# Kernel tuning notes

Hardware: AMD Instinct MI355X
Metric: run time of the kernel (lower is better)

The kernel has to match this reference:

```python
import jax, jax.numpy as jnp
import numpy as np

N_NODES = 100000
N_EDGES = 3200000
N_FEAT = 128
N_CLASSES = 8


def setup_inputs() -> dict:
    key = jax.random.key(0)
    ks = jax.random.split(key, 8)
    h = jax.random.normal(ks[0], (N_NODES, N_FEAT), dtype=jnp.float32)
    edge_index = jax.random.randint(ks[1], (2, N_EDGES), 0, N_NODES, dtype=jnp.int64)
    def lin(k, fi, fo):
        return jax.random.normal(k, (fi, fo), dtype=jnp.float32) / np.sqrt(fi)
    return {
        "h": h,
        "edge_index": edge_index,
        "W1": lin(ks[2], N_FEAT, 16), "b1": jnp.zeros((16,), jnp.float32),
        "W2": lin(ks[3], 16, 4),      "b2": jnp.zeros((4,), jnp.float32),
        "W3": lin(ks[4], 4, 2),      "b3": jnp.zeros((2,), jnp.float32),
        "Wc": lin(ks[5], 2, N_CLASSES), "bc": jnp.zeros((N_CLASSES,), jnp.float32),
    }


def _gcn_norm(edge_index, n_nodes):
    # PyG GCNConv: add self-loops, symmetric normalization deg^-1/2 A deg^-1/2
    loop = jnp.arange(n_nodes, dtype=edge_index.dtype)
    src = jnp.concatenate([edge_index[0], loop])  # [E+N]
    dst = jnp.concatenate([edge_index[1], loop])
    deg = jax.ops.segment_sum(jnp.ones_like(dst, dtype=jnp.float32), dst,
                              num_segments=n_nodes)
    dinv = jnp.where(deg > 0, jax.lax.rsqrt(deg), 0.0)
    norm = dinv[src] * dinv[dst]  # [E+N]
    return src, dst, norm


def _gcn_conv(x, W, b, src, dst, norm, n_nodes):
    xw = x @ W                                # [N, Fo] linear first (small Fo)
    msg = xw[src] * norm[:, None]             # gather + scale  [E+N, Fo]
    out = jax.ops.segment_sum(msg, dst, num_segments=n_nodes)  # scatter-add
    return out + b


def reference(h, edge_index, W1, b1, W2, b2, W3, b3, Wc, bc):
    n = h.shape[0]
    src, dst, norm = _gcn_norm(edge_index, n)
    h1 = jnp.tanh(_gcn_conv(h, W1, b1, src, dst, norm, n))
    h2 = jnp.tanh(_gcn_conv(h1, W2, b2, src, dst, norm, n))
    h3 = jnp.tanh(_gcn_conv(h2, W3, b3, src, dst, norm, n))
    out = h3 @ Wc + bc
    return (out, h3)
```

## Files before the change

kernel.cpp:

```cpp
#include <hip/hip_runtime.h>
#include <math.h>

#define N_NODES 100000
#define N_EDGES 3200000
#define NPB    256
#define NBUCK  ((N_NODES + NPB - 1) / NPB)
#define NBLKA  256
#define EPB    ((N_EDGES + NBLKA - 1) / NBLKA)
#define NB_BLK ((N_NODES + 255) / 256)

#define NEW_WS_WORDS (3u*N_NODES + N_EDGES + 3200000u + NBUCK*NBLKA + NBUCK + 2u)
#define NEW_WS_BYTES (NEW_WS_WORDS * 4u)
#define ATOMIC_WS_BYTES ((33u*N_NODES + 16u) * 4u)

__global__ void k_detect_i64(const int* __restrict__ ei_words, int* __restrict__ flag) {
    if (blockIdx.x == 0 && threadIdx.x == 0) {
        int allzero = 1;
        for (int i = 0; i < 64; i++)
            if (ei_words[2 * i + 1] != 0) allzero = 0;
        *flag = allzero;
    }
}

__device__ __forceinline__ unsigned load_idx(const int* p32, const long long* p64,
                                             int is64, int e) {
    return is64 ? (unsigned)(unsigned long long)p64[e] : (unsigned)p32[e];
}

__global__ __launch_bounds__(256) void k_bcount(const int* __restrict__ dst32,
                                                const long long* __restrict__ dst64,
                                                const int* __restrict__ flag,
                                                int* __restrict__ cmat) {
    __shared__ int lc[NBUCK];
    int t = threadIdx.x, blk = blockIdx.x;
    for (int i = t; i < NBUCK; i += 256) lc[i] = 0;
    __syncthreads();
    int is64 = *flag;
    int e0 = blk * EPB;
    int e1 = e0 + EPB; if (e1 > N_EDGES) e1 = N_EDGES;
    for (int e = e0 + t; e < e1; e += 256) {
        unsigned d = load_idx(dst32, dst64, is64, e);
        if (d < N_NODES) atomicAdd(&lc[d >> 8], 1);
    }
    __syncthreads();
    for (int b = t; b < NBUCK; b += 256) cmat[b * NBLKA + blk] = lc[b];
}

__global__ __launch_bounds__(256) void k_bsum(const int* __restrict__ cmat,
                                              int* __restrict__ bt) {
    int b = blockIdx.x, t = threadIdx.x;
    int v = cmat[b * NBLKA + t];
#pragma unroll
    for (int off = 32; off > 0; off >>= 1) v += __shfl_down(v, off, 64);
    __shared__ int s[4];
    if ((t & 63) == 0) s[t >> 6] = v;
    __syncthreads();
    if (t == 0) bt[b] = s[0] + s[1] + s[2] + s[3];
}

__global__ __launch_bounds__(512) void k_btscan(int* __restrict__ bt) {
    __shared__ int s[512];
    int t = threadIdx.x;
    s[t] = (t < NBUCK) ? bt[t] : 0;
    __syncthreads();
    for (int off = 1; off < 512; off <<= 1) {
        int v = (t >= off) ? s[t - off] : 0;
        __syncthreads();
        s[t] += v;
        __syncthreads();
    }
    if (t < NBUCK) bt[t] = (t == 0) ? 0 : s[t - 1];
    if (t == 0) bt[NBUCK] = s[NBUCK - 1];
}

__global__ __launch_bounds__(256) void k_boffs(int* __restrict__ cmat,
                                               const int* __restrict__ bt) {
    __shared__ int s[256];
    int b = blockIdx.x, t = threadIdx.x;
    int v0 = cmat[b * NBLKA + t];
    s[t] = v0;
    __syncthreads();
    for (int off = 1; off < 256; off <<= 1) {
        int v = (t >= off) ? s[t - off] : 0;
        __syncthreads();
        s[t] += v;
        __syncthreads();
    }
    cmat[b * NBLKA + t] = ((t == 0) ? 0 : s[t - 1]) + bt[b];
}

__global__ __launch_bounds__(256) void k_bscatter(const int* __restrict__ src32,
                                                  const long long* __restrict__ src64,
                                                  const int* __restrict__ dst32,
                                                  const long long* __restrict__ dst64,
                                                  const int* __restrict__ flag,
                                                  const int* __restrict__ cmat,
                                                  int* __restrict__ P) {
    __shared__ int cur[NBUCK];
    int t = threadIdx.x, blk = blockIdx.x;
    for (int i = t; i < NBUCK; i += 256) cur[i] = cmat[i * NBLKA + blk];
    __syncthreads();
    int is64 = *flag;
    int e0 = blk * EPB;
    int e1 = e0 + EPB; if (e1 > N_EDGES) e1 = N_EDGES;
    for (int e = e0 + t; e < e1; e += 256) {
        unsigned d = load_idx(dst32, dst64, is64, e);
        if (d < N_NODES) {
            unsigned s = load_idx(src32, src64, is64, e);
            int pos = atomicAdd(&cur[d >> 8], 1);
            P[pos] = (int)(((d & 255u) << 17) | (s & 0x1FFFFu));
        }
    }
}

__global__ __launch_bounds__(256) void k_bbuild(const int* __restrict__ P,
                                                const int* __restrict__ bt,
                                                int* __restrict__ adj,
                                                int* __restrict__ rowstart,
                                                int* __restrict__ rowend,
                                                float* __restrict__ dinv) {
    __shared__ int cnt[NPB];
    __shared__ int s[NPB];
    int b = blockIdx.x, t = threadIdx.x;
    int bo = bt[b], be = bt[b + 1];
    cnt[t] = 0;
    __syncthreads();
    for (int i = bo + t; i < be; i += 256) atomicAdd(&cnt[P[i] >> 17], 1);
    __syncthreads();
    s[t] = cnt[t];
    __syncthreads();
    for (int off = 1; off < 256; off <<= 1) {
        int v = (t >= off) ? s[t - off] : 0;
        __syncthreads();
        s[t] += v;
        __syncthreads();
    }
    int ex = (t == 0) ? 0 : s[t - 1];
    int node = b * NPB + t;
    if (node < N_NODES) {
        rowstart[node] = bo + ex;
        rowend[node]   = bo + ex + cnt[t];
        dinv[node]     = rsqrtf((float)cnt[t] + 1.0f);
    }
    __syncthreads();
    s[t] = ex;
    __syncthreads();
    for (int i = bo + t; i < be; i += 256) {
        int ent = P[i];
        int pos = bo + atomicAdd(&s[ent >> 17], 1);
        adj[pos] = ent & 0x1FFFF;
    }
}

__global__ __launch_bounds__(256) void k_gemm1(const float* __restrict__ h,
                                               const float* __restrict__ W,
                                               const float* __restrict__ dinv,
                                               float* __restrict__ xs,
                                               float* acc) {
    __shared__ float Wt[16 * 132];
    __shared__ float Hs[16 * 132];
    int tid = threadIdx.x;
    for (int i = tid; i < 2048; i += 256) {
        int k = i >> 4, f = i & 15;
        Wt[f * 132 + k] = W[i];
    }
    int nodeBase = blockIdx.x * 16;
    for (int i = tid; i < 512; i += 256) {
        int r = i >> 5, c = i & 31;
        float4 v = ((const float4*)(h + (size_t)(nodeBase + r) * 128))[c];
        *((float4*)&Hs[r * 132 + c * 4]) = v;
    }
    __syncthreads();
    int nl = tid >> 4;
    int f  = tid & 15;
    int n  = nodeBase + nl;
    const float* hr = &Hs[nl * 132];
    const float* wr = &Wt[f * 132];
    float s = 0.0f;
#pragma unroll
    for (int k = 0; k < 128; k++) s += hr[k] * wr[k];
    s *= dinv[n];
    xs[n * 16 + f]  = s;
    acc[n * 16 + f] = s;
}

template <int FI, int FO>
__global__ __launch_bounds__(256) void k_gemm_small(const float* __restrict__ x,
                                                    const float* __restrict__ W,
                                                    const float* __restrict__ dinv,
                                                    float* __restrict__ xs,
                                                    float* acc) {
    int i = blockIdx.x * 256 + threadIdx.x;
    if (i >= N_NODES * FO) return;
    int n = i / FO, f = i % FO;
    float s = 0.0f;
#pragma unroll
    for (int k = 0; k < FI; k++) s += x[n * FI + k] * W[k * FO + f];
    s *= dinv[n];
    xs[i] = s;
    acc[i] = s;
}

template <int F, int NL>
__global__ __launch_bounds__(256) void k_pull(const float* __restrict__ xs,
                                              const int* __restrict__ adj,
                                              const int* __restrict__ rowstart,
                                              const int* __restrict__ rowend,
                                              const float* __restrict__ dinv,
                                              const float* __restrict__ b,
                                              float* __restrict__ out) {
    constexpr int R = NL / F;
    int t = threadIdx.x;
    int g = t / NL, q = t % NL;
    int f = q % F,  k = q / F;
    int n = blockIdx.x * (256 / NL) + g;
    if (n >= N_NODES) return;
    int s0 = rowstart[n], e0 = rowend[n];
    float acc = 0.0f;
    for (int j = s0 + k; j < e0; j += R)
        acc += xs[adj[j] * F + f];
#pragma unroll
    for (int off = NL / 2; off >= F; off >>= 1)
        acc += __shfl_xor(acc, off, 64);
    if (k == 0) {
        acc += xs[n * F + f];
        out[n * F + f] = tanhf(dinv[n] * acc + b[f]);
    }
}

__global__ __launch_bounds__(256) void k_pull_final(const float* __restrict__ xs,
                                                    const int* __restrict__ adj,
                                                    const int* __restrict__ rowstart,
                                                    const int* __restrict__ rowend,
                                                    const float* __restrict__ dinv,
                                                    const float* __restrict__ b3,
                                                    const float* __restrict__ Wc,
                                                    const float* __restrict__ bc,
                                                    float* __restrict__ out,
                                                    float* __restrict__ h3out) {
    const int NL = 8;
    int t = threadIdx.x;
    int g = t / NL, q = t % NL;
    int f = q & 1, k = q >> 1;
    int n = blockIdx.x * (256 / NL) + g;
    if (n >= N_NODES) return;
    int s0 = rowstart[n], e0 = rowend[n];
    float acc = 0.0f;
    for (int j = s0 + k; j < e0; j += 4)
        acc += xs[adj[j] * 2 + f];
    acc += __shfl_xor(acc, 4, 64);
    acc += __shfl_xor(acc, 2, 64);
    float a = 0.0f;
    if (q < 2) {
        acc += xs[n * 2 + f];
        a = tanhf(dinv[n] * acc + b3[f]);
        h3out[2 * n + f] = a;
    }
    int wl = t & 63, gb = wl & ~7;
    float a0 = __shfl(a, gb, 64);
    float a1 = __shfl(a, gb + 1, 64);
    out[8 * n + q] = a0 * Wc[q] + a1 * Wc[8 + q] + bc[q];
}

template <int F>
__global__ __launch_bounds__(256) void k_scatter(const int* __restrict__ src32,
                                                 const long long* __restrict__ src64,
                                                 const int* __restrict__ dst32,
                                                 const long long* __restrict__ dst64,
                                                 const int* __restrict__ flag,
                                                 const float* __restrict__ xs,
                                                 float* __restrict__ acc) {
    long long gid = (long long)blockIdx.x * 256 + threadIdx.x;
    int e = (int)(gid / F), f = (int)(gid % F);
    if (e < N_EDGES) {
        int is64 = *flag;
        unsigned s = load_idx(src32, src64, is64, e);
        unsigned d = load_idx(dst32, dst64, is64, e);
        if (s < N_NODES && d < N_NODES)
            atomicAdd(&acc[d * F + f], xs[s * F + f]);
    }
}
__global__ __launch_bounds__(256) void k_deg_init(float* __restrict__ deg) {
    int i = blockIdx.x * 256 + threadIdx.x;
    if (i < N_NODES) deg[i] = 1.0f;
}
__global__ __launch_bounds__(256) void k_deg_count(const int* __restrict__ dst32,
                                                   const long long* __restrict__ dst64,
                                                   const int* __restrict__ flag,
                                                   float* __restrict__ deg) {
    int e = blockIdx.x * 256 + threadIdx.x;
    if (e < N_EDGES) {
        unsigned d = load_idx(dst32, dst64, *flag, e);
        if (d < N_NODES) atomicAdd(&deg[d], 1.0f);
    }
}
__global__ __launch_bounds__(256) void k_rsqrt(float* __restrict__ deg) {
    int i = blockIdx.x * 256 + threadIdx.x;
    if (i < N_NODES) deg[i] = rsqrtf(deg[i]);
}
template <int F>
__global__ __launch_bounds__(256) void k_finish(const float* __restrict__ acc,
                                                const float* __restrict__ dinv,
                                                const float* __restrict__ b,
                                                float* __restrict__ out) {
    int i = blockIdx.x * 256 + threadIdx.x;
    if (i >= N_NODES * F) return;
    int n = i / F, f = i % F;
    out[i] = tanhf(dinv[n] * acc[i] + b[f]);
}
__global__ __launch_bounds__(256) void k_final(const float* __restrict__ acc3,
                                               const float* __restrict__ dinv,
                                               const float* __restrict__ b3,
                                               const float* __restrict__ Wc,
                                               const float* __restrict__ bc,
                                               float* __restrict__ out,
                                               float* __restrict__ h3out) {
    int n = blockIdx.x * 256 + threadIdx.x;
    if (n >= N_NODES) return;
    float di = dinv[n];
    float a0 = tanhf(di * acc3[2 * n + 0] + b3[0]);
    float a1 = tanhf(di * acc3[2 * n + 1] + b3[1]);
    h3out[2 * n + 0] = a0;
    h3out[2 * n + 1] = a1;
#pragma unroll
    for (int c = 0; c < 8; c++)
        out[8 * n + c] = a0 * Wc[c] + a1 * Wc[8 + c] + bc[c];
}
__global__ __launch_bounds__(256) void k_zero_out(float* __restrict__ out, int n) {
    int i = blockIdx.x * 256 + threadIdx.x;
    if (i < n) out[i] = 0.0f;
}

extern "C" void kernel_launch(void* const* d_in, const int* in_sizes, int n_in,
                              void* d_out, int out_size, void* d_ws, size_t ws_size,
                              hipStream_t stream) {
    float* out = (float*)d_out;
    const float* h   = (const float*)d_in[0];
    const void*  ei  = d_in[1];
    const float* W1  = (const float*)d_in[2];
    const float* b1  = (const float*)d_in[3];
    const float* W2  = (const float*)d_in[4];
    const float* b2  = (const float*)d_in[5];
    const float* W3  = (const float*)d_in[6];
    const float* b3  = (const float*)d_in[7];
    const float* Wc  = (const float*)d_in[8];
    const float* bc  = (const float*)d_in[9];

    const int*       src32 = (const int*)ei;
    const int*       dst32 = src32 + N_EDGES;
    const long long* src64 = (const long long*)ei;
    const long long* dst64 = src64 + N_EDGES;

    float* h3out = out + 8 * N_NODES;
    const int NB_E = (N_EDGES + 255) / 256;

    if (d_ws != nullptr && ws_size >= NEW_WS_BYTES) {
        float* dinv    = (float*)d_ws;
        int* rowstart  = (int*)(dinv + N_NODES);
        int* rowend    = rowstart + N_NODES;
        int* adj       = rowend + N_NODES;
        int* S         = adj + N_EDGES;
        float* xs      = (float*)S;
        float* hbuf    = xs + 16 * N_NODES;
        int* P         = S;
        int* cmat      = S + 3200000;
        int* bt        = cmat + NBUCK * NBLKA;
        int* flag      = bt + NBUCK + 1;

        k_detect_i64<<<1, 64, 0, stream>>>(src32, flag);
        k_bcount<<<NBLKA, 256, 0, stream>>>(dst32, dst64, flag, cmat);
        k_bsum<<<NBUCK, 256, 0, stream>>>(cmat, bt);
        k_btscan<<<1, 512, 0, stream>>>(bt);
        k_boffs<<<NBUCK, 256, 0, stream>>>(cmat, bt);
        k_bscatter<<<NBLKA, 256, 0, stream>>>(src32, src64, dst32, dst64, flag, cmat, P);
        k_bbuild<<<NBUCK, 256, 0, stream>>>(P, bt, adj, rowstart, rowend, dinv);

        k_gemm1<<<N_NODES / 16, 256, 0, stream>>>(h, W1, dinv, xs, xs);
        k_pull<16, 64><<<(N_NODES * 64 + 255) / 256, 256, 0, stream>>>(
            xs, adj, rowstart, rowend, dinv, b1, hbuf);
        k_gemm_small<16, 4><<<(N_NODES * 4 + 255) / 256, 256, 0, stream>>>(hbuf, W2, dinv, xs, xs);
        k_pull<4, 16><<<(N_NODES * 16 + 255) / 256, 256, 0, stream>>>(
            xs, adj, rowstart, rowend, dinv, b2, hbuf);
        k_gemm_small<4, 2><<<(N_NODES * 2 + 255) / 256, 256, 0, stream>>>(hbuf, W3, dinv, xs, xs);
        k_pull_final<<<(N_NODES * 8 + 255) / 256, 256, 0, stream>>>(
            xs, adj, rowstart, rowend, dinv, b3, Wc, bc, out, h3out);
        return;
    }

    if (d_ws != nullptr && ws_size >= ATOMIC_WS_BYTES) {
        float* ws   = (float*)d_ws;
        float* dinv = ws;
        float* bufA = dinv + N_NODES;
        float* bufB = bufA + 16 * N_NODES;
        int*   flag = (int*)(bufB + 16 * N_NODES);
        float* xs1 = bufA, *acc1 = bufB, *h1 = bufA;
        float* xs2 = bufB, *acc2 = bufB + 4 * N_NODES, *h2 = bufA;
        float* xs3 = bufB, *acc3 = bufB + 2 * N_NODES;

        k_detect_i64<<<1, 64, 0, stream>>>(src32, flag);
        k_deg_init<<<NB_BLK, 256, 0, stream>>>(dinv);
        k_deg_count<<<NB_E, 256, 0, stream>>>(dst32, dst64, flag, dinv);
        k_rsqrt<<<NB_BLK, 256, 0, stream>>>(dinv);
        k_gemm1<<<N_NODES / 16, 256, 0, stream>>>(h, W1, dinv, xs1, acc1);
        k_scatter<16><<<(int)(((long long)N_EDGES * 16 + 255) / 256), 256, 0, stream>>>(
            src32, src64, dst32, dst64, flag, xs1, acc1);
        k_finish<16><<<(N_NODES * 16 + 255) / 256, 256, 0, stream>>>(acc1, dinv, b1, h1);
        k_gemm_small<16, 4><<<(N_NODES * 4 + 255) / 256, 256, 0, stream>>>(h1, W2, dinv, xs2, acc2);
        k_scatter<4><<<(int)(((long long)N_EDGES * 4 + 255) / 256), 256, 0, stream>>>(
            src32, src64, dst32, dst64, flag, xs2, acc2);
        k_finish<4><<<(N_NODES * 4 + 255) / 256, 256, 0, stream>>>(acc2, dinv, b2, h2);
        k_gemm_small<4, 2><<<(N_NODES * 2 + 255) / 256, 256, 0, stream>>>(h2, W3, dinv, xs3, acc3);
        k_scatter<2><<<(int)(((long long)N_EDGES * 2 + 255) / 256), 256, 0, stream>>>(
            src32, src64, dst32, dst64, flag, xs3, acc3);
        k_final<<<NB_BLK, 256, 0, stream>>>(acc3, dinv, b3, Wc, bc, out, h3out);
        return;
    }

    k_zero_out<<<(out_size + 255) / 256, 256, 0, stream>>>(out, out_size);
}
```

Measured before the change: 351.0 us.

## Replace CSR pull with bucketed shared-memory atomic aggregation over packed edges

Drops the per-node CSR build (rowstart/rowend/adj) and aggregates directly from the bucket-sorted packed edge list P. Each block owns 128 destination nodes and accumulates messages with LDS atomics. Layer-1 features are split into two 8-wide planes so the shared accumulator fits, and edge-index and P reads use nontemporal loads. This removes the second sort pass and the irregular row-length imbalance, at the cost of reading P several times (once per layer or plane) and contended LDS atomics.

Result: slower. 738.5 us (+110.4%).

```diff
diff --git a/kernel.cpp b/kernel.cpp
--- a/kernel.cpp
+++ b/kernel.cpp
@@ -3,14 +3,14 @@
 
 #define N_NODES 100000
 #define N_EDGES 3200000
-#define NPB    256
+#define NPB    128
 #define NBUCK  ((N_NODES + NPB - 1) / NPB)
 #define NBLKA  256
 #define EPB    ((N_EDGES + NBLKA - 1) / NBLKA)
 #define NB_BLK ((N_NODES + 255) / 256)
 
-#define NEW_WS_WORDS (3u*N_NODES + N_EDGES + 3200000u + NBUCK*NBLKA + NBUCK + 2u)
-#define NEW_WS_BYTES (NEW_WS_WORDS * 4u)
+#define MAIN_WS_WORDS (33u*N_NODES + N_EDGES + NBUCK*NBLKA + NBUCK + 2u)
+#define MAIN_WS_BYTES (MAIN_WS_WORDS * 4u)
 #define ATOMIC_WS_BYTES ((33u*N_NODES + 16u) * 4u)
 
 __global__ void k_detect_i64(const int* __restrict__ ei_words, int* __restrict__ flag) {
@@ -24,7 +24,8 @@
 
 __device__ __forceinline__ unsigned load_idx(const int* p32, const long long* p64,
                                              int is64, int e) {
-    return is64 ? (unsigned)(unsigned long long)p64[e] : (unsigned)p32[e];
+    return is64 ? (unsigned)(unsigned long long)__builtin_nontemporal_load(&p64[e])
+                : (unsigned)__builtin_nontemporal_load(&p32[e]);
 }
 
 __global__ __launch_bounds__(256) void k_bcount(const int* __restrict__ dst32,
@@ -36,11 +37,10 @@
     for (int i = t; i < NBUCK; i += 256) lc[i] = 0;
     __syncthreads();
     int is64 = *flag;
-    int e0 = blk * EPB;
-    int e1 = e0 + EPB; if (e1 > N_EDGES) e1 = N_EDGES;
+    int e0 = blk * EPB, e1 = e0 + EPB; if (e1 > N_EDGES) e1 = N_EDGES;
     for (int e = e0 + t; e < e1; e += 256) {
         unsigned d = load_idx(dst32, dst64, is64, e);
-        if (d < N_NODES) atomicAdd(&lc[d >> 8], 1);
+        if (d < N_NODES) atomicAdd(&lc[d >> 7], 1);
     }
     __syncthreads();
     for (int b = t; b < NBUCK; b += 256) cmat[b * NBLKA + blk] = lc[b];
@@ -58,12 +58,12 @@
     if (t == 0) bt[b] = s[0] + s[1] + s[2] + s[3];
 }
 
-__global__ __launch_bounds__(512) void k_btscan(int* __restrict__ bt) {
-    __shared__ int s[512];
+__global__ __launch_bounds__(1024) void k_btscan(int* __restrict__ bt) {
+    __shared__ int s[1024];
     int t = threadIdx.x;
     s[t] = (t < NBUCK) ? bt[t] : 0;
     __syncthreads();
-    for (int off = 1; off < 512; off <<= 1) {
+    for (int off = 1; off < 1024; off <<= 1) {
         int v = (t >= off) ? s[t - off] : 0;
         __syncthreads();
         s[t] += v;
@@ -77,8 +77,7 @@
                                                const int* __restrict__ bt) {
     __shared__ int s[256];
     int b = blockIdx.x, t = threadIdx.x;
-    int v0 = cmat[b * NBLKA + t];
-    s[t] = v0;
+    s[t] = cmat[b * NBLKA + t];
     __syncthreads();
     for (int off = 1; off < 256; off <<= 1) {
         int v = (t >= off) ? s[t - off] : 0;
@@ -101,62 +100,38 @@
     for (int i = t; i < NBUCK; i += 256) cur[i] = cmat[i * NBLKA + blk];
     __syncthreads();
     int is64 = *flag;
-    int e0 = blk * EPB;
-    int e1 = e0 + EPB; if (e1 > N_EDGES) e1 = N_EDGES;
+    int e0 = blk * EPB, e1 = e0 + EPB; if (e1 > N_EDGES) e1 = N_EDGES;
     for (int e = e0 + t; e < e1; e += 256) {
         unsigned d = load_idx(dst32, dst64, is64, e);
         if (d < N_NODES) {
             unsigned s = load_idx(src32, src64, is64, e);
-            int pos = atomicAdd(&cur[d >> 8], 1);
-            P[pos] = (int)(((d & 255u) << 17) | (s & 0x1FFFFu));
+            int pos = atomicAdd(&cur[d >> 7], 1);
+            P[pos] = (int)(((d & 127u) << 17) | (s & 0x1FFFFu));
         }
     }
 }
 
-__global__ __launch_bounds__(256) void k_bbuild(const int* __restrict__ P,
-                                                const int* __restrict__ bt,
-                                                int* __restrict__ adj,
-                                                int* __restrict__ rowstart,
-                                                int* __restrict__ rowend,
-                                                float* __restrict__ dinv) {
+__global__ __launch_bounds__(256) void k_bdinv(const int* __restrict__ P,
+                                               const int* __restrict__ bt,
+                                               float* __restrict__ dinv) {
     __shared__ int cnt[NPB];
-    __shared__ int s[NPB];
     int b = blockIdx.x, t = threadIdx.x;
-    int bo = bt[b], be = bt[b + 1];
-    cnt[t] = 0;
-    __syncthreads();
-    for (int i = bo + t; i < be; i += 256) atomicAdd(&cnt[P[i] >> 17], 1);
-    __syncthreads();
-    s[t] = cnt[t];
-    __syncthreads();
-    for (int off = 1; off < 256; off <<= 1) {
-        int v = (t >= off) ? s[t - off] : 0;
-        __syncthreads();
-        s[t] += v;
-        __syncthreads();
-    }
-    int ex = (t == 0) ? 0 : s[t - 1];
-    int node = b * NPB + t;
-    if (node < N_NODES) {
-        rowstart[node] = bo + ex;
-        rowend[node]   = bo + ex + cnt[t];
-        dinv[node]     = rsqrtf((float)cnt[t] + 1.0f);
-    }
-    __syncthreads();
-    s[t] = ex;
-    __syncthreads();
-    for (int i = bo + t; i < be; i += 256) {
-        int ent = P[i];
-        int pos = bo + atomicAdd(&s[ent >> 17], 1);
-        adj[pos] = ent & 0x1FFFF;
-    }
-}
-
-__global__ __launch_bounds__(256) void k_gemm1(const float* __restrict__ h,
-                                               const float* __restrict__ W,
-                                               const float* __restrict__ dinv,
-                                               float* __restrict__ xs,
-                                               float* acc) {
+    for (int i = t; i < NPB; i += 256) cnt[i] = 0;
+    __syncthreads();
+    int s0 = bt[b], s1 = bt[b + 1];
+    for (int j = s0 + t; j < s1; j += 256)
+        atomicAdd(&cnt[__builtin_nontemporal_load(&P[j]) >> 17], 1);
+    __syncthreads();
+    for (int i = t; i < NPB; i += 256) {
+        int n = b * NPB + i;
+        if (n < N_NODES) dinv[n] = rsqrtf((float)cnt[i] + 1.0f);
+    }
+}
+
+__global__ __launch_bounds__(256) void k_gemm1_p(const float* __restrict__ h,
+                                                 const float* __restrict__ W,
+                                                 const float* __restrict__ dinv,
+                                                 float* __restrict__ xs) {
     __shared__ float Wt[16 * 132];
     __shared__ float Hs[16 * 132];
     int tid = threadIdx.x;
@@ -171,25 +146,136 @@
         *((float4*)&Hs[r * 132 + c * 4]) = v;
     }
     __syncthreads();
-    int nl = tid >> 4;
-    int f  = tid & 15;
-    int n  = nodeBase + nl;
+    int nl = tid >> 4, f = tid & 15;
+    int n = nodeBase + nl;
     const float* hr = &Hs[nl * 132];
     const float* wr = &Wt[f * 132];
     float s = 0.0f;
 #pragma unroll
     for (int k = 0; k < 128; k++) s += hr[k] * wr[k];
     s *= dinv[n];
-    xs[n * 16 + f]  = s;
+    xs[(f >> 3) * (8 * N_NODES) + n * 8 + (f & 7)] = s;
+}
+
+template <int FI, int FO>
+__global__ __launch_bounds__(256) void k_gemm_smallp(const float* __restrict__ x,
+                                                     const float* __restrict__ W,
+                                                     const float* __restrict__ dinv,
+                                                     float* __restrict__ xs) {
+    int i = blockIdx.x * 256 + threadIdx.x;
+    if (i >= N_NODES * FO) return;
+    int n = i / FO, f = i % FO;
+    float s = 0.0f;
+#pragma unroll
+    for (int k = 0; k < FI; k++) s += x[n * FI + k] * W[k * FO + f];
+    xs[i] = s * dinv[n];
+}
+
+template <int F, int FTOT, int FOFF, int LOG>
+__global__ __launch_bounds__(256) void k_agg(const int* __restrict__ P,
+                                             const int* __restrict__ bt,
+                                             const float* __restrict__ xsp,
+                                             const float* __restrict__ dinv,
+                                             const float* __restrict__ bias,
+                                             float* __restrict__ out) {
+    __shared__ float acc[NPB * F];
+    int b = blockIdx.x, t = threadIdx.x;
+    for (int i = t; i < NPB * F; i += 256) acc[i] = 0.0f;
+    __syncthreads();
+    int s0 = bt[b], s1 = bt[b + 1];
+    int sub = t & (F - 1);
+    for (int j = s0 + (t >> LOG); j < s1; j += (256 >> LOG)) {
+        int ent = __builtin_nontemporal_load(&P[j]);
+        int src = ent & 0x1FFFF;
+        int dl  = ent >> 17;
+        atomicAdd(&acc[dl * F + sub], xsp[src * F + sub]);
+    }
+    __syncthreads();
+    for (int i = t; i < NPB * F; i += 256) {
+        int n = b * NPB + (i >> LOG);
+        if (n < N_NODES) {
+            int fl = i & (F - 1);
+            float a = acc[i] + xsp[n * F + fl];
+            out[n * FTOT + FOFF + fl] = tanhf(dinv[n] * a + bias[fl]);
+        }
+    }
+}
+
+__global__ __launch_bounds__(256) void k_agg_final(const int* __restrict__ P,
+                                                   const int* __restrict__ bt,
+                                                   const float* __restrict__ xsp,
+                                                   const float* __restrict__ dinv,
+                                                   const float* __restrict__ b3,
+                                                   const float* __restrict__ Wc,
+                                                   const float* __restrict__ bc,
+                                                   float* __restrict__ out,
+                                                   float* __restrict__ h3out) {
+    __shared__ float acc[NPB * 2];
+    __shared__ float h3s[NPB * 2];
+    int b = blockIdx.x, t = threadIdx.x;
+    for (int i = t; i < NPB * 2; i += 256) acc[i] = 0.0f;
+    __syncthreads();
+    int s0 = bt[b], s1 = bt[b + 1];
+    int sub = t & 1;
+    for (int j = s0 + (t >> 1); j < s1; j += 128) {
+        int ent = __builtin_nontemporal_load(&P[j]);
+        int src = ent & 0x1FFFF;
+        int dl  = ent >> 17;
+        atomicAdd(&acc[dl * 2 + sub], xsp[src * 2 + sub]);
+    }
+    __syncthreads();
+    for (int i = t; i < NPB * 2; i += 256) {
+        int n = b * NPB + (i >> 1);
+        if (n < N_NODES) {
+            int fl = i & 1;
+            float a = tanhf(dinv[n] * (acc[i] + xsp[n * 2 + fl]) + b3[fl]);
+            h3s[i] = a;
+            h3out[n * 2 + fl] = a;
+        }
+    }
+    __syncthreads();
+    for (int i = t; i < NPB * 8; i += 256) {
+        int ln = i >> 3, c = i & 7;
+        int n = b * NPB + ln;
+        if (n < N_NODES)
+            out[n * 8 + c] = h3s[ln * 2] * Wc[c] + h3s[ln * 2 + 1] * Wc[8 + c] + bc[c];
+    }
+}
+
+__global__ __launch_bounds__(256) void k_gemm1(const float* __restrict__ h,
+                                               const float* __restrict__ W,
+                                               const float* __restrict__ dinv,
+                                               float* __restrict__ xs, float* acc) {
+    __shared__ float Wt[16 * 132];
+    __shared__ float Hs[16 * 132];
+    int tid = threadIdx.x;
+    for (int i = tid; i < 2048; i += 256) {
+        int k = i >> 4, f = i & 15;
+        Wt[f * 132 + k] = W[i];
+    }
+    int nodeBase = blockIdx.x * 16;
+    for (int i = tid; i < 512; i += 256) {
+        int r = i >> 5, c = i & 31;
+        float4 v = ((const float4*)(h + (size_t)(nodeBase + r) * 128))[c];
+        *((float4*)&Hs[r * 132 + c * 4]) = v;
+    }
+    __syncthreads();
+    int nl = tid >> 4, f = tid & 15;
+    int n = nodeBase + nl;
+    const float* hr = &Hs[nl * 132];
+    const float* wr = &Wt[f * 132];
+    float s = 0.0f;
+#pragma unroll
+    for (int k = 0; k < 128; k++) s += hr[k] * wr[k];
+    s *= dinv[n];
+    xs[n * 16 + f] = s;
     acc[n * 16 + f] = s;
 }
-
 template <int FI, int FO>
 __global__ __launch_bounds__(256) void k_gemm_small(const float* __restrict__ x,
                                                     const float* __restrict__ W,
                                                     const float* __restrict__ dinv,
-                                                    float* __restrict__ xs,
-                                                    float* acc) {
+                                                    float* __restrict__ xs, float* acc) {
     int i = blockIdx.x * 256 + threadIdx.x;
     if (i >= N_NODES * FO) return;
     int n = i / FO, f = i % FO;
@@ -200,68 +286,6 @@
     xs[i] = s;
     acc[i] = s;
 }
-
-template <int F, int NL>
-__global__ __launch_bounds__(256) void k_pull(const float* __restrict__ xs,
-                                              const int* __restrict__ adj,
-                                              const int* __restrict__ rowstart,
-                                              const int* __restrict__ rowend,
-                                              const float* __restrict__ dinv,
-                                              const float* __restrict__ b,
-                                              float* __restrict__ out) {
-    constexpr int R = NL / F;
-    int t = threadIdx.x;
-    int g = t / NL, q = t % NL;
-    int f = q % F,  k = q / F;
-    int n = blockIdx.x * (256 / NL) + g;
-    if (n >= N_NODES) return;
-    int s0 = rowstart[n], e0 = rowend[n];
-    float acc = 0.0f;
-    for (int j = s0 + k; j < e0; j += R)
-        acc += xs[adj[j] * F + f];
-#pragma unroll
-    for (int off = NL / 2; off >= F; off >>= 1)
-        acc += __shfl_xor(acc, off, 64);
-    if (k == 0) {
-        acc += xs[n * F + f];
-        out[n * F + f] = tanhf(dinv[n] * acc + b[f]);
-    }
-}
-
-__global__ __launch_bounds__(256) void k_pull_final(const float* __restrict__ xs,
-                                                    const int* __restrict__ adj,
-                                                    const int* __restrict__ rowstart,
-                                                    const int* __restrict__ rowend,
-                                                    const float* __restrict__ dinv,
-                                                    const float* __restrict__ b3,
-                                                    const float* __restrict__ Wc,
-                                                    const float* __restrict__ bc,
-                                                    float* __restrict__ out,
-                                                    float* __restrict__ h3out) {
-    const int NL = 8;
-    int t = threadIdx.x;
-    int g = t / NL, q = t % NL;
-    int f = q & 1, k = q >> 1;
-    int n = blockIdx.x * (256 / NL) + g;
-    if (n >= N_NODES) return;
-    int s0 = rowstart[n], e0 = rowend[n];
-    float acc = 0.0f;
-    for (int j = s0 + k; j < e0; j += 4)
-        acc += xs[adj[j] * 2 + f];
-    acc += __shfl_xor(acc, 4, 64);
-    acc += __shfl_xor(acc, 2, 64);
-    float a = 0.0f;
-    if (q < 2) {
-        acc += xs[n * 2 + f];
-        a = tanhf(dinv[n] * acc + b3[f]);
-        h3out[2 * n + f] = a;
-    }
-    int wl = t & 63, gb = wl & ~7;
-    float a0 = __shfl(a, gb, 64);
-    float a1 = __shfl(a, gb + 1, 64);
-    out[8 * n + q] = a0 * Wc[q] + a1 * Wc[8 + q] + bc[q];
-}
-
 template <int F>
 __global__ __launch_bounds__(256) void k_scatter(const int* __restrict__ src32,
                                                  const long long* __restrict__ src64,
@@ -354,36 +378,30 @@
     float* h3out = out + 8 * N_NODES;
     const int NB_E = (N_EDGES + 255) / 256;
 
-    if (d_ws != nullptr && ws_size >= NEW_WS_BYTES) {
-        float* dinv    = (float*)d_ws;
-        int* rowstart  = (int*)(dinv + N_NODES);
-        int* rowend    = rowstart + N_NODES;
-        int* adj       = rowend + N_NODES;
-        int* S         = adj + N_EDGES;
-        float* xs      = (float*)S;
-        float* hbuf    = xs + 16 * N_NODES;
-        int* P         = S;
-        int* cmat      = S + 3200000;
-        int* bt        = cmat + NBUCK * NBLKA;
-        int* flag      = bt + NBUCK + 1;
+    if (d_ws != nullptr && ws_size >= MAIN_WS_BYTES) {
+        float* dinv = (float*)d_ws;
+        float* xs   = dinv + N_NODES;
+        float* hbuf = xs + 16 * N_NODES;
+        int*   P    = (int*)(hbuf + 16 * N_NODES);
+        int*   cmat = P + N_EDGES;
+        int*   bt   = cmat + NBUCK * NBLKA;
+        int*   flag = bt + NBUCK + 1;
 
         k_detect_i64<<<1, 64, 0, stream>>>(src32, flag);
         k_bcount<<<NBLKA, 256, 0, stream>>>(dst32, dst64, flag, cmat);
         k_bsum<<<NBUCK, 256, 0, stream>>>(cmat, bt);
-        k_btscan<<<1, 512, 0, stream>>>(bt);
+        k_btscan<<<1, 1024, 0, stream>>>(bt);
         k_boffs<<<NBUCK, 256, 0, stream>>>(cmat, bt);
         k_bscatter<<<NBLKA, 256, 0, stream>>>(src32, src64, dst32, dst64, flag, cmat, P);
-        k_bbuild<<<NBUCK, 256, 0, stream>>>(P, bt, adj, rowstart, rowend, dinv);
-
-        k_gemm1<<<N_NODES / 16, 256, 0, stream>>>(h, W1, dinv, xs, xs);
-        k_pull<16, 64><<<(N_NODES * 64 + 255) / 256, 256, 0, stream>>>(
-            xs, adj, rowstart, rowend, dinv, b1, hbuf);
-        k_gemm_small<16, 4><<<(N_NODES * 4 + 255) / 256, 256, 0, stream>>>(hbuf, W2, dinv, xs, xs);
-        k_pull<4, 16><<<(N_NODES * 16 + 255) / 256, 256, 0, stream>>>(
-            xs, adj, rowstart, rowend, dinv, b2, hbuf);
-        k_gemm_small<4, 2><<<(N_NODES * 2 + 255) / 256, 256, 0, stream>>>(hbuf, W3, dinv, xs, xs);
-        k_pull_final<<<(N_NODES * 8 + 255) / 256, 256, 0, stream>>>(
-            xs, adj, rowstart, rowend, dinv, b3, Wc, bc, out, h3out);
+        k_bdinv<<<NBUCK, 256, 0, stream>>>(P, bt, dinv);
+
+        k_gemm1_p<<<N_NODES / 16, 256, 0, stream>>>(h, W1, dinv, xs);
+        k_agg<8, 16, 0, 3><<<NBUCK, 256, 0, stream>>>(P, bt, xs, dinv, b1, hbuf);
+        k_agg<8, 16, 8, 3><<<NBUCK, 256, 0, stream>>>(P, bt, xs + 8 * N_NODES, dinv, b1 + 8, hbuf);
+        k_gemm_smallp<16, 4><<<(N_NODES * 4 + 255) / 256, 256, 0, stream>>>(hbuf, W2, dinv, xs);
+        k_agg<4, 4, 0, 2><<<NBUCK, 256, 0, stream>>>(P, bt, xs, dinv, b2, hbuf);
+        k_gemm_smallp<4, 2><<<(N_NODES * 2 + 255) / 256, 256, 0, stream>>>(hbuf, W3, dinv, xs);
+        k_agg_final<<<NBUCK, 256, 0, stream>>>(P, bt, xs, dinv, b3, Wc, bc, out, h3out);
         return;
     }
 
```
